# Kernel tuning notes

Hardware: AMD Instinct MI355X
Metric: run time of the kernel (lower is better)

The kernel has to match this reference:

```python
import jax, jax.numpy as jnp
import numpy as np

G = 128          # number of point-cloud groups
DOWNSAMPLE = 256 # points per group
D = 256          # feature dim


def _pairwise_dist(x, y):
    # x: [G, n, d], y: [G, m, d] -> Euclidean distances [G, n, m]
    x2 = jnp.sum(x * x, axis=-1)[:, :, None]
    y2 = jnp.sum(y * y, axis=-1)[:, None, :]
    d2 = jnp.maximum(x2 + y2 - 2.0 * jnp.einsum('gnd,gmd->gnm', x, y), 0.0)
    # safe sqrt (zero diagonal has zero distance, avoid NaN grads)
    return jnp.where(d2 > 0, jnp.sqrt(jnp.where(d2 > 0, d2, 1.0)), 0.0)


def setup_inputs() -> dict:
    key = jax.random.key(0)
    k1, k2 = jax.random.split(key)
    inp = jax.random.normal(k1, (G * DOWNSAMPLE, D), dtype=jnp.float32)
    tgt = jax.random.normal(k2, (G * DOWNSAMPLE, D), dtype=jnp.float32)
    return {"input": inp, "target": tgt, "downsample": DOWNSAMPLE}


def reference(input, target, downsample):
    # MMDLoss.forward: reshape to (-1, downsample, D), batched energy distance, mean
    x = input.reshape(-1, downsample, input.shape[-1])   # [G, n, D]
    y = target.reshape(-1, downsample, target.shape[-1]) # [G, m, D]
    # Energy distance (geomloss 'energy' kernel k(x,y) = -||x-y||, uniform weights):
    # L = mean_ij ||x_i - y_j|| - 0.5 mean_ij ||x_i - x_j|| - 0.5 mean_ij ||y_i - y_j||
    d_xy = jnp.mean(_pairwise_dist(x, y), axis=(1, 2))  # [G]
    d_xx = jnp.mean(_pairwise_dist(x, x), axis=(1, 2))  # [G]
    d_yy = jnp.mean(_pairwise_dist(y, y), axis=(1, 2))  # [G]
    loss_per_group = d_xy - 0.5 * d_xx - 0.5 * d_yy
    return jnp.mean(loss_per_group)
```

## Files before the change

kernel.cpp:

```cpp
#include <hip/hip_runtime.h>
#include <stdint.h>

typedef __attribute__((ext_vector_type(8))) short short8;
typedef __attribute__((ext_vector_type(4))) float floatx4;

#define NPTS 256
#define DIM  256
#define TILE 128
#define BK   32
#define LDSS 40

static __device__ __forceinline__ uint16_t bf16_rne(float f) {
    uint32_t u = __builtin_bit_cast(uint32_t, f);
    u += 0x7FFFu + ((u >> 16) & 1u);
    return (uint16_t)(u >> 16);
}
static __device__ __forceinline__ float bf16f(uint16_t h) {
    uint32_t u = ((uint32_t)h) << 16;
    return __builtin_bit_cast(float, u);
}
static __device__ __forceinline__ float trunc_bf16f(float f) {
    uint32_t u = __builtin_bit_cast(uint32_t, f) & 0xFFFF0000u;
    return __builtin_bit_cast(float, u);
}
static __device__ __forceinline__ uint32_t pack_trunc(float a, float b) {
    uint32_t ua = __builtin_bit_cast(uint32_t, a);
    uint32_t ub = __builtin_bit_cast(uint32_t, b);
    return (ua >> 16) | (ub & 0xFFFF0000u);
}

template<bool BIG>
__global__ __launch_bounds__(256)
void mmd_norms(const float* __restrict__ X, const float* __restrict__ Y,
               float* __restrict__ x2, float* __restrict__ y2,
               uint16_t* __restrict__ Xb, uint16_t* __restrict__ Yb, int npts) {
    int lane = threadIdx.x & 63;
    int wv   = threadIdx.x >> 6;
    int pblk = blockIdx.x * 16;
    #pragma unroll
    for (int r = 0; r < 4; ++r) {
        int p = pblk + wv + 4 * r;
        const float* src; float* dst; uint16_t* bdst; int pl;
        if (p < npts) { src = X; dst = x2; bdst = Xb; pl = p; }
        else          { src = Y; dst = y2; bdst = Yb; pl = p - npts; }
        const float4 v = *(const float4*)(src + (size_t)pl * DIM + lane * 4);
        float f0, f1, f2, f3;
        if (BIG) {
            uint16_t b0 = bf16_rne(v.x), b1 = bf16_rne(v.y),
                     b2 = bf16_rne(v.z), b3 = bf16_rne(v.w);
            f0 = bf16f(b0); f1 = bf16f(b1); f2 = bf16f(b2); f3 = bf16f(b3);
            ushort4 pk = { b0, b1, b2, b3 };
            *(ushort4*)(bdst + (size_t)pl * DIM + lane * 4) = pk;
        } else {
            f0 = trunc_bf16f(v.x); f1 = trunc_bf16f(v.y);
            f2 = trunc_bf16f(v.z); f3 = trunc_bf16f(v.w);
        }
        float ssq = f0 * f0 + f1 * f1 + f2 * f2 + f3 * f3;
        #pragma unroll
        for (int off = 32; off; off >>= 1) ssq += __shfl_down(ssq, off);
        if (lane == 0) dst[pl] = ssq;
    }
}

template<bool FROM_BF16>
__global__ __launch_bounds__(256)
void mmd_gemm(const float* __restrict__ X, const float* __restrict__ Y,
              const uint16_t* __restrict__ Xb, const uint16_t* __restrict__ Yb,
              const float* __restrict__ x2, const float* __restrict__ y2,
              float* __restrict__ out, float scale) {
    int g = blockIdx.y;
    int t = blockIdx.x;

    int ptype, ti, tj; float w;
    if (t < 4)      { ptype = 0; ti = t >> 1; tj = t & 1; w = 1.0f; }
    else if (t < 7) { int u = t - 4; ptype = 1; ti = (u == 2); tj = (u >= 1); w = (u == 1) ? -1.0f : -0.5f; }
    else            { int u = t - 7; ptype = 2; ti = (u == 2); tj = (u >= 1); w = (u == 1) ? -1.0f : -0.5f; }

    const float *Pf, *Qf, *rn_g, *cn_g;
    const uint16_t *Pb, *Qb;
    if (ptype == 0)      { Pf = X; Qf = Y; Pb = Xb; Qb = Yb; rn_g = x2; cn_g = y2; }
    else if (ptype == 1) { Pf = X; Qf = X; Pb = Xb; Qb = Xb; rn_g = x2; cn_g = x2; }
    else                 { Pf = Y; Qf = Y; Pb = Yb; Qb = Yb; rn_g = y2; cn_g = y2; }
    const bool symdiag = (ptype != 0) && (ti == tj);

    const size_t prow0 = (size_t)g * NPTS + (size_t)ti * TILE;
    const size_t qrow0 = (size_t)g * NPTS + (size_t)tj * TILE;

    __shared__ uint16_t As[TILE * LDSS];
    __shared__ uint16_t Bs[TILE * LDSS];
    __shared__ float rnorm[TILE];
    __shared__ float cnorm[TILE];
    __shared__ float wpart[4];

    const int tid  = threadIdx.x;
    const int lane = tid & 63;
    const int wv   = tid >> 6;
    const int wrow = (wv >> 1) * 64;
    const int wcol = (wv & 1) * 64;
    const int quad = lane >> 4;
    const int l15  = lane & 15;

    floatx4 acc[4][4];
    #pragma unroll
    for (int i = 0; i < 4; ++i)
        #pragma unroll
        for (int j = 0; j < 4; ++j) acc[i][j] = (floatx4)0.0f;

    for (int kk = 0; kk < DIM; kk += BK) {
        __syncthreads();
        if (FROM_BF16) {
            #pragma unroll
            for (int i = 0; i < 2; ++i) {
                int gg = tid + i * 256;
                int row = gg >> 2, c0 = (gg & 3) * 8;
                *(short8*)&As[row * LDSS + c0] =
                    *(const short8*)(Pb + (prow0 + row) * DIM + kk + c0);
                *(short8*)&Bs[row * LDSS + c0] =
                    *(const short8*)(Qb + (qrow0 + row) * DIM + kk + c0);
            }
        } else {
            #pragma unroll
            for (int i = 0; i < 4; ++i) {
                int f = tid + i * 256;
                int row = f >> 3, c0 = (f & 7) * 4;
                float4 v = *(const float4*)(Pf + (prow0 + row) * DIM + kk + c0);
                uint2 pk = { pack_trunc(v.x, v.y), pack_trunc(v.z, v.w) };
                *(uint2*)&As[row * LDSS + c0] = pk;
                v = *(const float4*)(Qf + (qrow0 + row) * DIM + kk + c0);
                uint2 pk2 = { pack_trunc(v.x, v.y), pack_trunc(v.z, v.w) };
                *(uint2*)&Bs[row * LDSS + c0] = pk2;
            }
        }
        __syncthreads();

        short8 af[4], bfr[4];
        #pragma unroll
        for (int mi = 0; mi < 4; ++mi)
            af[mi] = *(const short8*)&As[(wrow + mi * 16 + l15) * LDSS + quad * 8];
        #pragma unroll
        for (int ni = 0; ni < 4; ++ni)
            bfr[ni] = *(const short8*)&Bs[(wcol + ni * 16 + l15) * LDSS + quad * 8];
        #pragma unroll
        for (int mi = 0; mi < 4; ++mi)
            #pragma unroll
            for (int ni = 0; ni < 4; ++ni)
                acc[mi][ni] = __builtin_amdgcn_mfma_f32_16x16x32_bf16(
                    af[mi], bfr[ni], acc[mi][ni], 0, 0, 0);
    }

    __syncthreads();
    if (tid < TILE) rnorm[tid] = rn_g[prow0 + tid];
    else            cnorm[tid - TILE] = cn_g[qrow0 + tid - TILE];
    __syncthreads();

    float lsum = 0.0f;
    #pragma unroll
    for (int mi = 0; mi < 4; ++mi) {
        #pragma unroll
        for (int i = 0; i < 4; ++i) {
            int r = wrow + mi * 16 + quad * 4 + i;
            float rv = rnorm[r];
            #pragma unroll
            for (int ni = 0; ni < 4; ++ni) {
                int c = wcol + ni * 16 + l15;
                float d2 = rv + cnorm[c] - 2.0f * acc[mi][ni][i];
                d2 = fmaxf(d2, 0.0f);
                float s = sqrtf(d2);
                if (symdiag && (r == c)) s = 0.0f;
                lsum += s;
            }
        }
    }
    #pragma unroll
    for (int off = 32; off; off >>= 1) lsum += __shfl_down(lsum, off);
    if (lane == 0) wpart[wv] = lsum;
    __syncthreads();
    if (tid == 0) {
        float bs = wpart[0] + wpart[1] + wpart[2] + wpart[3];
        atomicAdd(out, bs * (w * scale));
    }
}

extern "C" void kernel_launch(void* const* d_in, const int* in_sizes, int n_in,
                              void* d_out, int out_size, void* d_ws, size_t ws_size,
                              hipStream_t stream) {
    const float* X = (const float*)d_in[0];
    const float* Y = (const float*)d_in[1];
    const int total_elems = in_sizes[0];
    const int npts = total_elems / DIM;
    const int G = npts / NPTS;

    float* x2 = (float*)d_ws;
    float* y2 = x2 + npts;
    uint16_t* Xb = (uint16_t*)(y2 + npts);
    uint16_t* Yb = Xb + (size_t)total_elems;

    const size_t need_big = (size_t)npts * 2 * sizeof(float)
                          + (size_t)total_elems * 2 * sizeof(uint16_t);
    const bool big = ws_size >= need_big;

    float* out = (float*)d_out;
    hipMemsetAsync(out, 0, sizeof(float) * out_size, stream);

    const int nblk = (2 * npts) / 16;
    if (big) mmd_norms<true ><<<nblk, 256, 0, stream>>>(X, Y, x2, y2, Xb, Yb, npts);
    else     mmd_norms<false><<<nblk, 256, 0, stream>>>(X, Y, x2, y2, Xb, Yb, npts);

    const float scale = 1.0f / ((float)NPTS * (float)NPTS * (float)G);
    dim3 grid(10, G);
    if (big) mmd_gemm<true ><<<grid, 256, 0, stream>>>(X, Y, Xb, Yb, x2, y2, out, scale);
    else     mmd_gemm<false><<<grid, 256, 0, stream>>>(X, Y, Xb, Yb, x2, y2, out, scale);
}
```

Before: 137.4 us.

## Fuse norm and bf16 conversion into GEMM kernel with larger K tiles

Removes the separate norms/bf16-conversion kernel. Each GEMM block now reads fp32 inputs directly, rounds them to bf16 while staging into LDS, and computes the row norms on the fly. The K tile grows from 32 to 128, so there are only two LDS stages per block. This saves a launch and a workspace write/read pass. In exchange, fp32 data is re-read by several tiles, LDS use is much larger (about 70KB), which may limit occupancy, and each block does redundant conversion and norm work.

```diff
diff --git a/kernel.cpp b/kernel.cpp
--- a/kernel.cpp
+++ b/kernel.cpp
@@ -7,80 +7,33 @@
 #define NPTS 256
 #define DIM  256
 #define TILE 128
-#define BK   32
-#define LDSS 40
+#define BK   128
+#define LDSS 136
 
-static __device__ __forceinline__ uint16_t bf16_rne(float f) {
+static __device__ __forceinline__ uint32_t rne_hi(float f) {
     uint32_t u = __builtin_bit_cast(uint32_t, f);
     u += 0x7FFFu + ((u >> 16) & 1u);
-    return (uint16_t)(u >> 16);
+    return u & 0xFFFF0000u;
 }
-static __device__ __forceinline__ float bf16f(uint16_t h) {
-    uint32_t u = ((uint32_t)h) << 16;
-    return __builtin_bit_cast(float, u);
-}
-static __device__ __forceinline__ float trunc_bf16f(float f) {
-    uint32_t u = __builtin_bit_cast(uint32_t, f) & 0xFFFF0000u;
-    return __builtin_bit_cast(float, u);
-}
-static __device__ __forceinline__ uint32_t pack_trunc(float a, float b) {
-    uint32_t ua = __builtin_bit_cast(uint32_t, a);
-    uint32_t ub = __builtin_bit_cast(uint32_t, b);
-    return (ua >> 16) | (ub & 0xFFFF0000u);
+static __device__ __forceinline__ float hi_val(uint32_t hi) {
+    return __builtin_bit_cast(float, hi);
 }
 
-template<bool BIG>
 __global__ __launch_bounds__(256)
-void mmd_norms(const float* __restrict__ X, const float* __restrict__ Y,
-               float* __restrict__ x2, float* __restrict__ y2,
-               uint16_t* __restrict__ Xb, uint16_t* __restrict__ Yb, int npts) {
-    int lane = threadIdx.x & 63;
-    int wv   = threadIdx.x >> 6;
-    int pblk = blockIdx.x * 16;
-    #pragma unroll
-    for (int r = 0; r < 4; ++r) {
-        int p = pblk + wv + 4 * r;
-        const float* src; float* dst; uint16_t* bdst; int pl;
-        if (p < npts) { src = X; dst = x2; bdst = Xb; pl = p; }
-        else          { src = Y; dst = y2; bdst = Yb; pl = p - npts; }
-        const float4 v = *(const float4*)(src + (size_t)pl * DIM + lane * 4);
-        float f0, f1, f2, f3;
-        if (BIG) {
-            uint16_t b0 = bf16_rne(v.x), b1 = bf16_rne(v.y),
-                     b2 = bf16_rne(v.z), b3 = bf16_rne(v.w);
-            f0 = bf16f(b0); f1 = bf16f(b1); f2 = bf16f(b2); f3 = bf16f(b3);
-            ushort4 pk = { b0, b1, b2, b3 };
-            *(ushort4*)(bdst + (size_t)pl * DIM + lane * 4) = pk;
-        } else {
-            f0 = trunc_bf16f(v.x); f1 = trunc_bf16f(v.y);
-            f2 = trunc_bf16f(v.z); f3 = trunc_bf16f(v.w);
-        }
-        float ssq = f0 * f0 + f1 * f1 + f2 * f2 + f3 * f3;
-        #pragma unroll
-        for (int off = 32; off; off >>= 1) ssq += __shfl_down(ssq, off);
-        if (lane == 0) dst[pl] = ssq;
-    }
-}
-
-template<bool FROM_BF16>
-__global__ __launch_bounds__(256)
-void mmd_gemm(const float* __restrict__ X, const float* __restrict__ Y,
-              const uint16_t* __restrict__ Xb, const uint16_t* __restrict__ Yb,
-              const float* __restrict__ x2, const float* __restrict__ y2,
-              float* __restrict__ out, float scale) {
-    int g = blockIdx.y;
-    int t = blockIdx.x;
+void mmd_fused(const float* __restrict__ X, const float* __restrict__ Y,
+               float* __restrict__ out, float scale) {
+    const int g = blockIdx.y;
+    const int t = blockIdx.x;
 
     int ptype, ti, tj; float w;
     if (t < 4)      { ptype = 0; ti = t >> 1; tj = t & 1; w = 1.0f; }
     else if (t < 7) { int u = t - 4; ptype = 1; ti = (u == 2); tj = (u >= 1); w = (u == 1) ? -1.0f : -0.5f; }
     else            { int u = t - 7; ptype = 2; ti = (u == 2); tj = (u >= 1); w = (u == 1) ? -1.0f : -0.5f; }
 
-    const float *Pf, *Qf, *rn_g, *cn_g;
-    const uint16_t *Pb, *Qb;
-    if (ptype == 0)      { Pf = X; Qf = Y; Pb = Xb; Qb = Yb; rn_g = x2; cn_g = y2; }
-    else if (ptype == 1) { Pf = X; Qf = X; Pb = Xb; Qb = Xb; rn_g = x2; cn_g = x2; }
-    else                 { Pf = Y; Qf = Y; Pb = Yb; Qb = Yb; rn_g = y2; cn_g = y2; }
+    const float *Pf, *Qf;
+    if (ptype == 0)      { Pf = X; Qf = Y; }
+    else if (ptype == 1) { Pf = X; Qf = X; }
+    else                 { Pf = Y; Qf = Y; }
     const bool symdiag = (ptype != 0) && (ti == tj);
 
     const size_t prow0 = (size_t)g * NPTS + (size_t)ti * TILE;
@@ -106,66 +59,76 @@
         #pragma unroll
         for (int j = 0; j < 4; ++j) acc[i][j] = (floatx4)0.0f;
 
-    for (int kk = 0; kk < DIM; kk += BK) {
-        __syncthreads();
-        if (FROM_BF16) {
+    #pragma unroll
+    for (int iter = 0; iter < 2; ++iter) {
+        const int kk = iter * BK;
+        if (iter) __syncthreads();
+
+        #pragma unroll
+        for (int i = 0; i < 16; ++i) {
+            const int f   = tid + i * 256;
+            const int row = f >> 5;
+            const int c4  = (f & 31) << 2;
+
+            const float4 vp = *(const float4*)(Pf + (prow0 + row) * DIM + kk + c4);
+            const float4 vq = *(const float4*)(Qf + (qrow0 + row) * DIM + kk + c4);
+
+            uint32_t p0 = rne_hi(vp.x), p1 = rne_hi(vp.y), p2 = rne_hi(vp.z), p3 = rne_hi(vp.w);
+            uint32_t q0 = rne_hi(vq.x), q1 = rne_hi(vq.y), q2 = rne_hi(vq.z), q3 = rne_hi(vq.w);
+
+            uint2 pp = { (p0 >> 16) | p1, (p2 >> 16) | p3 };
+            uint2 qq = { (q0 >> 16) | q1, (q2 >> 16) | q3 };
+            *(uint2*)&As[row * LDSS + c4] = pp;
+            *(uint2*)&Bs[row * LDSS + c4] = qq;
+
+            float a0 = hi_val(p0), a1 = hi_val(p1), a2 = hi_val(p2), a3 = hi_val(p3);
+            float b0 = hi_val(q0), b1 = hi_val(q1), b2 = hi_val(q2), b3 = hi_val(q3);
+            float sp = a0 * a0 + a1 * a1 + a2 * a2 + a3 * a3;
+            float sq = b0 * b0 + b1 * b1 + b2 * b2 + b3 * b3;
+
             #pragma unroll
-            for (int i = 0; i < 2; ++i) {
-                int gg = tid + i * 256;
-                int row = gg >> 2, c0 = (gg & 3) * 8;
-                *(short8*)&As[row * LDSS + c0] =
-                    *(const short8*)(Pb + (prow0 + row) * DIM + kk + c0);
-                *(short8*)&Bs[row * LDSS + c0] =
-                    *(const short8*)(Qb + (qrow0 + row) * DIM + kk + c0);
+            for (int off = 16; off; off >>= 1) {
+                sp += __shfl_down(sp, off);
+                sq += __shfl_down(sq, off);
             }
-        } else {
-            #pragma unroll
-            for (int i = 0; i < 4; ++i) {
-                int f = tid + i * 256;
-                int row = f >> 3, c0 = (f & 7) * 4;
-                float4 v = *(const float4*)(Pf + (prow0 + row) * DIM + kk + c0);
-                uint2 pk = { pack_trunc(v.x, v.y), pack_trunc(v.z, v.w) };
-                *(uint2*)&As[row * LDSS + c0] = pk;
-                v = *(const float4*)(Qf + (qrow0 + row) * DIM + kk + c0);
-                uint2 pk2 = { pack_trunc(v.x, v.y), pack_trunc(v.z, v.w) };
-                *(uint2*)&Bs[row * LDSS + c0] = pk2;
+            if ((lane & 31) == 0) {
+                if (iter == 0) { rnorm[row] = sp;  cnorm[row] = sq; }
+                else           { rnorm[row] += sp; cnorm[row] += sq; }
             }
         }
         __syncthreads();
 
-        short8 af[4], bfr[4];
         #pragma unroll
-        for (int mi = 0; mi < 4; ++mi)
-            af[mi] = *(const short8*)&As[(wrow + mi * 16 + l15) * LDSS + quad * 8];
-        #pragma unroll
-        for (int ni = 0; ni < 4; ++ni)
-            bfr[ni] = *(const short8*)&Bs[(wcol + ni * 16 + l15) * LDSS + quad * 8];
-        #pragma unroll
-        for (int mi = 0; mi < 4; ++mi)
+        for (int ks = 0; ks < 4; ++ks) {
+            const int kof = ks * 32 + quad * 8;
+            short8 af[4], bfr[4];
+            #pragma unroll
+            for (int mi = 0; mi < 4; ++mi)
+                af[mi] = *(const short8*)&As[(wrow + mi * 16 + l15) * LDSS + kof];
             #pragma unroll
             for (int ni = 0; ni < 4; ++ni)
-                acc[mi][ni] = __builtin_amdgcn_mfma_f32_16x16x32_bf16(
-                    af[mi], bfr[ni], acc[mi][ni], 0, 0, 0);
+                bfr[ni] = *(const short8*)&Bs[(wcol + ni * 16 + l15) * LDSS + kof];
+            #pragma unroll
+            for (int mi = 0; mi < 4; ++mi)
+                #pragma unroll
+                for (int ni = 0; ni < 4; ++ni)
+                    acc[mi][ni] = __builtin_amdgcn_mfma_f32_16x16x32_bf16(
+                        af[mi], bfr[ni], acc[mi][ni], 0, 0, 0);
+        }
     }
-
-    __syncthreads();
-    if (tid < TILE) rnorm[tid] = rn_g[prow0 + tid];
-    else            cnorm[tid - TILE] = cn_g[qrow0 + tid - TILE];
-    __syncthreads();
 
     float lsum = 0.0f;
     #pragma unroll
     for (int mi = 0; mi < 4; ++mi) {
         #pragma unroll
         for (int i = 0; i < 4; ++i) {
-            int r = wrow + mi * 16 + quad * 4 + i;
-            float rv = rnorm[r];
+            const int r = wrow + mi * 16 + quad * 4 + i;
+            const float rv = rnorm[r];
             #pragma unroll
             for (int ni = 0; ni < 4; ++ni) {
-                int c = wcol + ni * 16 + l15;
+                const int c = wcol + ni * 16 + l15;
                 float d2 = rv + cnorm[c] - 2.0f * acc[mi][ni][i];
-                d2 = fmaxf(d2, 0.0f);
-                float s = sqrtf(d2);
+                float s = sqrtf(fmaxf(d2, 0.0f));
                 if (symdiag && (r == c)) s = 0.0f;
                 lsum += s;
             }
@@ -187,27 +150,12 @@
     const float* X = (const float*)d_in[0];
     const float* Y = (const float*)d_in[1];
     const int total_elems = in_sizes[0];
-    const int npts = total_elems / DIM;
-    const int G = npts / NPTS;
-
-    float* x2 = (float*)d_ws;
-    float* y2 = x2 + npts;
-    uint16_t* Xb = (uint16_t*)(y2 + npts);
-    uint16_t* Yb = Xb + (size_t)total_elems;
-
-    const size_t need_big = (size_t)npts * 2 * sizeof(float)
-                          + (size_t)total_elems * 2 * sizeof(uint16_t);
-    const bool big = ws_size >= need_big;
+    const int G = total_elems / (NPTS * DIM);
 
     float* out = (float*)d_out;
     hipMemsetAsync(out, 0, sizeof(float) * out_size, stream);
 
-    const int nblk = (2 * npts) / 16;
-    if (big) mmd_norms<true ><<<nblk, 256, 0, stream>>>(X, Y, x2, y2, Xb, Yb, npts);
-    else     mmd_norms<false><<<nblk, 256, 0, stream>>>(X, Y, x2, y2, Xb, Yb, npts);
-
     const float scale = 1.0f / ((float)NPTS * (float)NPTS * (float)G);
     dim3 grid(10, G);
-    if (big) mmd_gemm<true ><<<grid, 256, 0, stream>>>(X, Y, Xb, Yb, x2, y2, out, scale);
-    else     mmd_gemm<false><<<grid, 256, 0, stream>>>(X, Y, Xb, Yb, x2, y2, out, scale);
+    mmd_fused<<<grid, 256, 0, stream>>>(X, Y, out, scale);
 }
```

Measured after the change: 207.2 us. +50.8%, slower.

## Use direct global-to-LDS loads with double-buffered tiles in bf16 GEMM path

Applied to the files above, without the earlier changes.

The bf16 GEMM path now copies tiles straight from global memory into LDS with the global_load_lds builtin instead of going through registers. It adds a double buffer so the next K slice is fetched while MFMAs run on the current one, and it loads the norms before the main loop. The LDS layout loses its padding (row stride 32 instead of 40), which may cause bank conflicts on the fragment reads. The fp32 fallback kernel stays as it was, split out into its own function.

```diff
diff --git a/kernel.cpp b/kernel.cpp
--- a/kernel.cpp
+++ b/kernel.cpp
@@ -27,6 +27,13 @@
     uint32_t ua = __builtin_bit_cast(uint32_t, a);
     uint32_t ub = __builtin_bit_cast(uint32_t, b);
     return (ua >> 16) | (ub & 0xFFFF0000u);
+}
+
+static __device__ __forceinline__ void gl2lds16(const void* gsrc, void* ldst) {
+    __builtin_amdgcn_global_load_lds(
+        (const __attribute__((address_space(1))) unsigned int*)gsrc,
+        (__attribute__((address_space(3))) unsigned int*)ldst,
+        16, 0, 0);
 }
 
 template<bool BIG>
@@ -62,32 +69,31 @@
     }
 }
 
-template<bool FROM_BF16>
-__global__ __launch_bounds__(256)
-void mmd_gemm(const float* __restrict__ X, const float* __restrict__ Y,
-              const uint16_t* __restrict__ Xb, const uint16_t* __restrict__ Yb,
-              const float* __restrict__ x2, const float* __restrict__ y2,
-              float* __restrict__ out, float scale) {
-    int g = blockIdx.y;
-    int t = blockIdx.x;
-
-    int ptype, ti, tj; float w;
+static __device__ __forceinline__ void tile_decode(int t, int& ptype, int& ti, int& tj, float& w) {
     if (t < 4)      { ptype = 0; ti = t >> 1; tj = t & 1; w = 1.0f; }
     else if (t < 7) { int u = t - 4; ptype = 1; ti = (u == 2); tj = (u >= 1); w = (u == 1) ? -1.0f : -0.5f; }
     else            { int u = t - 7; ptype = 2; ti = (u == 2); tj = (u >= 1); w = (u == 1) ? -1.0f : -0.5f; }
-
-    const float *Pf, *Qf, *rn_g, *cn_g;
-    const uint16_t *Pb, *Qb;
-    if (ptype == 0)      { Pf = X; Qf = Y; Pb = Xb; Qb = Yb; rn_g = x2; cn_g = y2; }
-    else if (ptype == 1) { Pf = X; Qf = X; Pb = Xb; Qb = Xb; rn_g = x2; cn_g = x2; }
-    else                 { Pf = Y; Qf = Y; Pb = Yb; Qb = Yb; rn_g = y2; cn_g = y2; }
+}
+
+__global__ __launch_bounds__(256)
+void mmd_gemm_dma(const uint16_t* __restrict__ Xb, const uint16_t* __restrict__ Yb,
+                  const float* __restrict__ x2, const float* __restrict__ y2,
+                  float* __restrict__ out, float scale) {
+    const int g = blockIdx.y;
+    int ptype, ti, tj; float w;
+    tile_decode(blockIdx.x, ptype, ti, tj, w);
+
+    const uint16_t *Pb, *Qb; const float *rn_g, *cn_g;
+    if (ptype == 0)      { Pb = Xb; Qb = Yb; rn_g = x2; cn_g = y2; }
+    else if (ptype == 1) { Pb = Xb; Qb = Xb; rn_g = x2; cn_g = x2; }
+    else                 { Pb = Yb; Qb = Yb; rn_g = y2; cn_g = y2; }
     const bool symdiag = (ptype != 0) && (ti == tj);
 
     const size_t prow0 = (size_t)g * NPTS + (size_t)ti * TILE;
     const size_t qrow0 = (size_t)g * NPTS + (size_t)tj * TILE;
 
-    __shared__ uint16_t As[TILE * LDSS];
-    __shared__ uint16_t Bs[TILE * LDSS];
+    __shared__ uint16_t As[2][TILE * BK];
+    __shared__ uint16_t Bs[2][TILE * BK];
     __shared__ float rnorm[TILE];
     __shared__ float cnorm[TILE];
     __shared__ float wpart[4];
@@ -100,6 +106,114 @@
     const int quad = lane >> 4;
     const int l15  = lane & 15;
 
+    if (tid < TILE) rnorm[tid] = rn_g[prow0 + tid];
+    else            cnorm[tid - TILE] = cn_g[qrow0 + tid - TILE];
+
+    const int r0a  = wv * 32;
+    const int srow = lane >> 2;
+    const int scol = (lane & 3) << 3;
+    const uint16_t* pA = Pb + (prow0 + r0a + srow) * DIM + scol;
+    const uint16_t* pB = Qb + (qrow0 + r0a + srow) * DIM + scol;
+
+    floatx4 acc[4][4];
+    #pragma unroll
+    for (int i = 0; i < 4; ++i)
+        #pragma unroll
+        for (int j = 0; j < 4; ++j) acc[i][j] = (floatx4)0.0f;
+
+    {
+        gl2lds16(pA,            &As[0][(r0a     ) * BK]);
+        gl2lds16(pA + 16 * DIM, &As[0][(r0a + 16) * BK]);
+        gl2lds16(pB,            &Bs[0][(r0a     ) * BK]);
+        gl2lds16(pB + 16 * DIM, &Bs[0][(r0a + 16) * BK]);
+    }
+
+    #pragma unroll
+    for (int it = 0; it < DIM / BK; ++it) {
+        const int b = it & 1;
+        __syncthreads();
+
+        if (it < DIM / BK - 1) {
+            const int kk = (it + 1) * BK;
+            gl2lds16(pA + kk,            &As[b ^ 1][(r0a     ) * BK]);
+            gl2lds16(pA + 16 * DIM + kk, &As[b ^ 1][(r0a + 16) * BK]);
+            gl2lds16(pB + kk,            &Bs[b ^ 1][(r0a     ) * BK]);
+            gl2lds16(pB + 16 * DIM + kk, &Bs[b ^ 1][(r0a + 16) * BK]);
+        }
+
+        short8 af[4], bfr[4];
+        #pragma unroll
+        for (int mi = 0; mi < 4; ++mi)
+            af[mi] = *(const short8*)&As[b][(wrow + mi * 16 + l15) * BK + quad * 8];
+        #pragma unroll
+        for (int ni = 0; ni < 4; ++ni)
+            bfr[ni] = *(const short8*)&Bs[b][(wcol + ni * 16 + l15) * BK + quad * 8];
+        #pragma unroll
+        for (int mi = 0; mi < 4; ++mi)
+            #pragma unroll
+            for (int ni = 0; ni < 4; ++ni)
+                acc[mi][ni] = __builtin_amdgcn_mfma_f32_16x16x32_bf16(
+                    af[mi], bfr[ni], acc[mi][ni], 0, 0, 0);
+    }
+
+    float lsum = 0.0f;
+    #pragma unroll
+    for (int mi = 0; mi < 4; ++mi) {
+        #pragma unroll
+        for (int i = 0; i < 4; ++i) {
+            const int r = wrow + mi * 16 + quad * 4 + i;
+            const float rv = rnorm[r];
+            #pragma unroll
+            for (int ni = 0; ni < 4; ++ni) {
+                const int c = wcol + ni * 16 + l15;
+                float d2 = rv + cnorm[c] - 2.0f * acc[mi][ni][i];
+                float s = sqrtf(fmaxf(d2, 0.0f));
+                if (symdiag && (r == c)) s = 0.0f;
+                lsum += s;
+            }
+        }
+    }
+    #pragma unroll
+    for (int off = 32; off; off >>= 1) lsum += __shfl_down(lsum, off);
+    if (lane == 0) wpart[wv] = lsum;
+    __syncthreads();
+    if (tid == 0) {
+        float bs = wpart[0] + wpart[1] + wpart[2] + wpart[3];
+        atomicAdd(out, bs * (w * scale));
+    }
+}
+
+__global__ __launch_bounds__(256)
+void mmd_gemm_fb(const float* __restrict__ X, const float* __restrict__ Y,
+                 const float* __restrict__ x2, const float* __restrict__ y2,
+                 float* __restrict__ out, float scale) {
+    const int g = blockIdx.y;
+    int ptype, ti, tj; float w;
+    tile_decode(blockIdx.x, ptype, ti, tj, w);
+
+    const float *Pf, *Qf, *rn_g, *cn_g;
+    if (ptype == 0)      { Pf = X; Qf = Y; rn_g = x2; cn_g = y2; }
+    else if (ptype == 1) { Pf = X; Qf = X; rn_g = x2; cn_g = x2; }
+    else                 { Pf = Y; Qf = Y; rn_g = y2; cn_g = y2; }
+    const bool symdiag = (ptype != 0) && (ti == tj);
+
+    const size_t prow0 = (size_t)g * NPTS + (size_t)ti * TILE;
+    const size_t qrow0 = (size_t)g * NPTS + (size_t)tj * TILE;
+
+    __shared__ uint16_t As[TILE * LDSS];
+    __shared__ uint16_t Bs[TILE * LDSS];
+    __shared__ float rnorm[TILE];
+    __shared__ float cnorm[TILE];
+    __shared__ float wpart[4];
+
+    const int tid  = threadIdx.x;
+    const int lane = tid & 63;
+    const int wv   = tid >> 6;
+    const int wrow = (wv >> 1) * 64;
+    const int wcol = (wv & 1) * 64;
+    const int quad = lane >> 4;
+    const int l15  = lane & 15;
+
     floatx4 acc[4][4];
     #pragma unroll
     for (int i = 0; i < 4; ++i)
@@ -108,28 +222,16 @@
 
     for (int kk = 0; kk < DIM; kk += BK) {
         __syncthreads();
-        if (FROM_BF16) {
-            #pragma unroll
-            for (int i = 0; i < 2; ++i) {
-                int gg = tid + i * 256;
-                int row = gg >> 2, c0 = (gg & 3) * 8;
-                *(short8*)&As[row * LDSS + c0] =
-                    *(const short8*)(Pb + (prow0 + row) * DIM + kk + c0);
-                *(short8*)&Bs[row * LDSS + c0] =
-                    *(const short8*)(Qb + (qrow0 + row) * DIM + kk + c0);
-            }
-        } else {
-            #pragma unroll
-            for (int i = 0; i < 4; ++i) {
-                int f = tid + i * 256;
-                int row = f >> 3, c0 = (f & 7) * 4;
-                float4 v = *(const float4*)(Pf + (prow0 + row) * DIM + kk + c0);
-                uint2 pk = { pack_trunc(v.x, v.y), pack_trunc(v.z, v.w) };
-                *(uint2*)&As[row * LDSS + c0] = pk;
-                v = *(const float4*)(Qf + (qrow0 + row) * DIM + kk + c0);
-                uint2 pk2 = { pack_trunc(v.x, v.y), pack_trunc(v.z, v.w) };
-                *(uint2*)&Bs[row * LDSS + c0] = pk2;
-            }
+        #pragma unroll
+        for (int i = 0; i < 4; ++i) {
+            int f = tid + i * 256;
+            int row = f >> 3, c0 = (f & 7) * 4;
+            float4 v = *(const float4*)(Pf + (prow0 + row) * DIM + kk + c0);
+            uint2 pk = { pack_trunc(v.x, v.y), pack_trunc(v.z, v.w) };
+            *(uint2*)&As[row * LDSS + c0] = pk;
+            v = *(const float4*)(Qf + (qrow0 + row) * DIM + kk + c0);
+            uint2 pk2 = { pack_trunc(v.x, v.y), pack_trunc(v.z, v.w) };
+            *(uint2*)&Bs[row * LDSS + c0] = pk2;
         }
         __syncthreads();
 
@@ -164,8 +266,7 @@
             for (int ni = 0; ni < 4; ++ni) {
                 int c = wcol + ni * 16 + l15;
                 float d2 = rv + cnorm[c] - 2.0f * acc[mi][ni][i];
-                d2 = fmaxf(d2, 0.0f);
-                float s = sqrtf(d2);
+                float s = sqrtf(fmaxf(d2, 0.0f));
                 if (symdiag && (r == c)) s = 0.0f;
                 lsum += s;
             }
@@ -208,6 +309,6 @@
 
     const float scale = 1.0f / ((float)NPTS * (float)NPTS * (float)G);
     dim3 grid(10, G);
-    if (big) mmd_gemm<true ><<<grid, 256, 0, stream>>>(X, Y, Xb, Yb, x2, y2, out, scale);
-    else     mmd_gemm<false><<<grid, 256, 0, stream>>>(X, Y, Xb, Yb, x2, y2, out, scale);
-}
+    if (big) mmd_gemm_dma<<<grid, 256, 0, stream>>>(Xb, Yb, x2, y2, out, scale);
+    else     mmd_gemm_fb <<<grid, 256, 0, stream>>>(X, Y, x2, y2, out, scale);
+}
```

Result: no change. 137.9 us (+0.4%).
